# Kernel tuning notes

Measured on AMD Instinct MI355X. Metric: run time of the kernel, lower is better.

The kernel has to match this reference:

```python
import jax, jax.numpy as jnp
import numpy as np

N, E = 30000, 480000
IN_DIM, HID, HEADS, OUT_DIM, EDIM = 128, 64, 4, 32, 1
NEG_SLOPE = 0.2
EPS_BN = 1e-5


def segment_softmax(logits, seg, num_segments):
    m = jax.ops.segment_max(logits, seg, num_segments=num_segments)
    ex = jnp.exp(logits - m[seg])
    s = jax.ops.segment_sum(ex, seg, num_segments=num_segments)
    return ex / (s[seg] + 1e-16)


def gat_layer(x, src, dst, ea, W, We, a_s, a_d, a_e, b):
    # PyG GATConv: shared lin for src/dst, edge_dim attention, softmax over dst
    n = x.shape[0]
    H, D = a_s.shape
    h = (x @ W).reshape(n, H, D)                      # [N,H,D]
    e = (ea @ We).reshape(-1, H, D)                   # [E,H,D]
    logits = (h * a_s).sum(-1)[src] + (h * a_d).sum(-1)[dst] + (e * a_e).sum(-1)
    alpha = segment_softmax(jax.nn.leaky_relu(logits, NEG_SLOPE), dst, n)  # [E,H]
    out = jax.ops.segment_sum(alpha[:, :, None] * h[src], dst, num_segments=n)
    return out.reshape(n, H * D) + b


def setup_inputs() -> dict:
    key = jax.random.key(0)
    ks = jax.random.split(key, 24)
    s = 0.1
    return {
        "x": jax.random.normal(ks[0], (N, IN_DIM), jnp.float32),
        "edge_attr": jax.random.uniform(ks[1], (E, EDIM), jnp.float32),
        "bn_gamma": jnp.ones((EDIM,), jnp.float32),
        "bn_beta": jnp.zeros((EDIM,), jnp.float32),
        "W1": s * jax.random.normal(ks[2], (IN_DIM, HEADS * HID), jnp.float32),
        "We1": s * jax.random.normal(ks[3], (EDIM, HEADS * HID), jnp.float32),
        "a_src1": s * jax.random.normal(ks[4], (HEADS, HID), jnp.float32),
        "a_dst1": s * jax.random.normal(ks[5], (HEADS, HID), jnp.float32),
        "a_edge1": s * jax.random.normal(ks[6], (HEADS, HID), jnp.float32),
        "b1": jnp.zeros((HEADS * HID,), jnp.float32),
        "W2": s * jax.random.normal(ks[7], (HEADS * HID, OUT_DIM), jnp.float32),
        "We2": s * jax.random.normal(ks[8], (EDIM, OUT_DIM), jnp.float32),
        "a_src2": s * jax.random.normal(ks[9], (1, OUT_DIM), jnp.float32),
        "a_dst2": s * jax.random.normal(ks[10], (1, OUT_DIM), jnp.float32),
        "a_edge2": s * jax.random.normal(ks[11], (1, OUT_DIM), jnp.float32),
        "b2": jnp.zeros((OUT_DIM,), jnp.float32),
        "dec_W1": s * jax.random.normal(ks[12], (OUT_DIM, HID), jnp.float32),
        "dec_b1": jnp.zeros((HID,), jnp.float32),
        "dec_W2": s * jax.random.normal(ks[13], (HID, IN_DIM), jnp.float32),
        "dec_b2": jnp.zeros((IN_DIM,), jnp.float32),
        "edge_index": jax.random.randint(ks[14], (2, E), 0, N, dtype=jnp.int32),
    }


def reference(x, edge_attr, bn_gamma, bn_beta, W1, We1, a_src1, a_dst1, a_edge1, b1,
              W2, We2, a_src2, a_dst2, a_edge2, b2, dec_W1, dec_b1, dec_W2, dec_b2,
              edge_index):
    n = x.shape[0]
    src, dst = edge_index[0], edge_index[1]
    # BatchNorm1d (batch stats, biased var) on log1p(edge_attr)
    ea = jnp.log1p(edge_attr)
    mu = ea.mean(0)
    var = ea.var(0)
    ea = (ea - mu) / jnp.sqrt(var + EPS_BN) * bn_gamma + bn_beta
    # add_self_loops with fill_value='mean' (mean of incoming edge attrs per node)
    ones = jnp.ones((src.shape[0],), ea.dtype)
    cnt = jax.ops.segment_sum(ones, dst, num_segments=n)
    loop_attr = jax.ops.segment_sum(ea, dst, num_segments=n) / jnp.maximum(cnt, 1.0)[:, None]
    ar = jnp.arange(n)
    src2 = jnp.concatenate([src, ar])
    dst2 = jnp.concatenate([dst, ar])
    ea2 = jnp.concatenate([ea, loop_attr], axis=0)
    # encoder: 2-layer GAT (eval mode: dropout is identity)
    h = jax.nn.elu(gat_layer(x, src2, dst2, ea2, W1, We1, a_src1, a_dst1, a_edge1, b1))
    z = gat_layer(h, src2, dst2, ea2, W2, We2, a_src2, a_dst2, a_edge2, b2)
    # feature decoder MLP
    x_hat = jax.nn.elu(z @ dec_W1 + dec_b1) @ dec_W2 + dec_b2
    return z, x_hat
```

## Files before the change

### kernel.cpp

```cpp
#include <hip/hip_runtime.h>
#include <math.h>

#define NN 30000
#define EE 480000
#define NEG_SLOPE 0.2f
#define LDK 136
#define LDK2 264
#define CAP 48
#define NPB 1875
#define NGB 938
#define EAQ 32767.0f
#define LN2V 0.6931472f

static const size_t I_FILL  = 0;
static const size_t F_PART  = 30000;
static const size_t F_SCAL  = 34096;
static const size_t F_WTB   = 34112;
static const size_t F_WT2B  = 50496;
static const size_t F_HB    = 54592;
static const size_t F_S1    = 3894592;
static const size_t F_D1    = 4014592;
static const size_t F_H1B   = 4134592;
static const size_t F_H2    = 7974592;
static const size_t F_S2    = 8934592;
static const size_t F_D2    = 8964592;
static const size_t I_ER    = 8994592;

typedef __attribute__((ext_vector_type(4))) float f32x4;
typedef __attribute__((ext_vector_type(8))) short bf16x8;

__device__ __forceinline__ float wsum64(float v) {
    #pragma unroll
    for (int o = 32; o; o >>= 1) v += __shfl_xor(v, o);
    return v;
}
__device__ __forceinline__ unsigned int pack_bf2(float a, float b) {
    unsigned int ua = __float_as_uint(a);
    unsigned int ub = __float_as_uint(b);
    ua = (ua + 0x7FFFu + ((ua >> 16) & 1u)) >> 16;
    ub = (ub + 0x7FFFu + ((ub >> 16) & 1u)) & 0xFFFF0000u;
    return ua | ub;
}
__device__ __forceinline__ unsigned short bf16r(float f) {
    unsigned int u = __float_as_uint(f);
    u = (u + 0x7FFFu + ((u >> 16) & 1u)) >> 16;
    return (unsigned short)u;
}
__device__ __forceinline__ float bflo(unsigned int u) { return __uint_as_float(u << 16); }
__device__ __forceinline__ float bfhi(unsigned int u) { return __uint_as_float(u & 0xFFFF0000u); }

__global__ __launch_bounds__(256) void k_prepw(const float* __restrict__ W1,
        const float* __restrict__ W2, unsigned short* __restrict__ wtb,
        unsigned short* __restrict__ wt2b, int* __restrict__ fill) {
    int idx = blockIdx.x * 256 + threadIdx.x;
    if (idx < NN) fill[idx] = 0;
    if (idx < 128 * 256) {
        int k = idx >> 8, n = idx & 255;
        wtb[n * 128 + k] = bf16r(W1[idx]);
    } else if (idx < 128 * 256 + 256 * 32) {
        int i2 = idx - 128 * 256;
        int k = i2 >> 5, c = i2 & 31;
        wt2b[c * 256 + k] = bf16r(W2[i2]);
    }
}

__global__ __launch_bounds__(256) void k_scat_gemm(const int* __restrict__ src,
        const int* __restrict__ dst, const float* __restrict__ eattr,
        int* __restrict__ fill, unsigned int* __restrict__ er,
        float* __restrict__ part,
        const float* __restrict__ x, const unsigned short* __restrict__ wtb,
        const float* __restrict__ as1, const float* __restrict__ ad1,
        unsigned short* __restrict__ hb, float* __restrict__ s1,
        float* __restrict__ d1, int E, int M) {
    __shared__ char shbuf[32 * LDK * 2];
    int tid = threadIdx.x;

    if (blockIdx.x < NPB) {
        float* sa = (float*)shbuf;
        float* sb = sa + 256;
        int e = blockIdx.x * 256 + tid;
        float s = 0.f, s2 = 0.f;
        if (e < E) {
            float lv = log1pf(eattr[e]);
            s = lv; s2 = lv * lv;
            int d = dst[e];
            int pos = atomicAdd(&fill[d], 1);
            if (pos > CAP - 2) pos = CAP - 2;
            unsigned int q = (unsigned int)(lv * (EAQ / LN2V) + 0.5f);
            if (q > 32767u) q = 32767u;
            er[d * CAP + pos] = ((unsigned int)src[e] << 15) | q;
        }
        sa[tid] = s; sb[tid] = s2;
        __syncthreads();
        for (int o = 128; o; o >>= 1) {
            if (tid < o) { sa[tid] += sa[tid + o]; sb[tid] += sb[tid + o]; }
            __syncthreads();
        }
        if (tid == 0) { part[blockIdx.x * 2] = sa[0]; part[blockIdx.x * 2 + 1] = sb[0]; }
        return;
    }

    unsigned short* xs = (unsigned short*)shbuf;
    int bm = (blockIdx.x - NPB) * 32;
    #pragma unroll
    for (int i = 0; i < 4; i++) {
        int idx = tid + i * 256;
        int row = idx >> 5, c4 = (idx & 31) * 4;
        int grow = bm + row;
        float4 v = make_float4(0.f, 0.f, 0.f, 0.f);
        if (grow < M) v = *(const float4*)&x[grow * 128 + c4];
        uint2 p = make_uint2(pack_bf2(v.x, v.y), pack_bf2(v.z, v.w));
        *(uint2*)&xs[row * LDK + c4] = p;
    }
    __syncthreads();

    int w = tid >> 6;
    int l = tid & 63;
    int l15 = l & 15, lg = l >> 4;

    f32x4 acc[2][4];
    #pragma unroll
    for (int m = 0; m < 2; m++)
        #pragma unroll
        for (int n = 0; n < 4; n++) acc[m][n] = (f32x4){0.f, 0.f, 0.f, 0.f};

    #pragma unroll
    for (int ks = 0; ks < 4; ks++) {
        int k0 = ks * 32 + lg * 8;
        bf16x8 a0 = *(const bf16x8*)&xs[(l15) * LDK + k0];
        bf16x8 a1 = *(const bf16x8*)&xs[(16 + l15) * LDK + k0];
        bf16x8 b[4];
        #pragma unroll
        for (int n = 0; n < 4; n++)
            b[n] = *(const bf16x8*)&wtb[(w * 64 + n * 16 + l15) * 128 + k0];
        #pragma unroll
        for (int n = 0; n < 4; n++) {
            acc[0][n] = __builtin_amdgcn_mfma_f32_16x16x32_bf16(a0, b[n], acc[0][n], 0, 0, 0);
            acc[1][n] = __builtin_amdgcn_mfma_f32_16x16x32_bf16(a1, b[n], acc[1][n], 0, 0, 0);
        }
    }

    #pragma unroll
    for (int m = 0; m < 2; m++) {
        #pragma unroll
        for (int r = 0; r < 4; r++) {
            int grow = bm + m * 16 + lg * 4 + r;
            if (grow < M) {
                #pragma unroll
                for (int n = 0; n < 4; n++)
                    hb[grow * 256 + w * 64 + n * 16 + l15] = bf16r(acc[m][n][r]);
            }
        }
    }
    float as_c[4], ad_c[4];
    #pragma unroll
    for (int n = 0; n < 4; n++) {
        as_c[n] = as1[w * 64 + n * 16 + l15];
        ad_c[n] = ad1[w * 64 + n * 16 + l15];
    }
    float sp[2][4], dp[2][4];
    #pragma unroll
    for (int m = 0; m < 2; m++)
        #pragma unroll
        for (int r = 0; r < 4; r++) {
            float s = 0.f, d = 0.f;
            #pragma unroll
            for (int n = 0; n < 4; n++) {
                s += acc[m][n][r] * as_c[n];
                d += acc[m][n][r] * ad_c[n];
            }
            sp[m][r] = s; dp[m][r] = d;
        }
    #pragma unroll
    for (int o = 1; o < 16; o <<= 1) {
        #pragma unroll
        for (int m = 0; m < 2; m++)
            #pragma unroll
            for (int r = 0; r < 4; r++) {
                sp[m][r] += __shfl_xor(sp[m][r], o);
                dp[m][r] += __shfl_xor(dp[m][r], o);
            }
    }
    if (l15 == 0) {
        #pragma unroll
        for (int m = 0; m < 2; m++)
            #pragma unroll
            for (int r = 0; r < 4; r++) {
                int grow = bm + m * 16 + lg * 4 + r;
                if (grow < M) {
                    s1[grow * 4 + w] = sp[m][r];
                    d1[grow * 4 + w] = dp[m][r];
                }
            }
    }
}

__global__ __launch_bounds__(512) void k_bn_final(const float* __restrict__ part,
        const float* __restrict__ gamma, const float* __restrict__ beta,
        const float* __restrict__ We1, const float* __restrict__ ae1,
        const float* __restrict__ We2, const float* __restrict__ ae2,
        float* __restrict__ scal, int E) {
    __shared__ float sa[512], sb[512], sc[256];
    int tid = threadIdx.x;
    float s = 0.f, s2 = 0.f;
    for (int i = tid; i < NPB; i += 512) {
        s += part[2 * i]; s2 += part[2 * i + 1];
    }
    sa[tid] = s; sb[tid] = s2;
    if (tid < 256) sc[tid] = We1[tid] * ae1[tid];
    __syncthreads();
    for (int o = 256; o; o >>= 1) {
        if (tid < o) { sa[tid] += sa[tid + o]; sb[tid] += sb[tid + o]; }
        __syncthreads();
    }
    if (tid == 0) {
        float mu = sa[0] / (float)E;
        float var = sb[0] / (float)E - mu * mu;
        float kA = gamma[0] / sqrtf(var + 1e-5f);
        float kB = beta[0] - mu * kA;
        for (int h = 0; h < 4; h++) {
            float s1 = 0.f;
            for (int d = 0; d < 64; d++) s1 += sc[h * 64 + d];
            scal[4 + h] = kA * s1;
            scal[10 + h] = kB * s1;
        }
        float s22 = 0.f;
        for (int d = 0; d < 32; d++) s22 += We2[d] * ae2[d];
        scal[8] = kA * s22;
        scal[9] = kB * s22;
    }
}

__global__ __launch_bounds__(256) void k_agg1(const int* __restrict__ fill,
        const unsigned int* __restrict__ er, const float* __restrict__ s1,
        const float* __restrict__ d1, const float* __restrict__ scal,
        const unsigned short* __restrict__ hb, const float* __restrict__ b1,
        unsigned short* __restrict__ h1b, int N) {
    __shared__ float sma[4][256];
    __shared__ int   sms[4][64];
    int wid = threadIdx.x >> 6;
    int node = blockIdx.x * 4 + wid;
    if (node >= N) return;
    int lane = threadIdx.x & 63;
    int deg = fill[node]; if (deg > CAP - 1) deg = CAP - 1;
    float4 dv = *(const float4*)&d1[node * 4];
    float4 ce = *(const float4*)&scal[4];
    float4 cc = *(const float4*)&scal[10];

    unsigned int rec = (unsigned int)node << 15;
    if (lane < deg) rec = er[node * CAP + lane];
    unsigned int sidx = rec >> 15;
    float ev = (float)(rec & 32767u) * (LN2V / EAQ);
    if (lane >= deg) ev = 0.f;
    float evm = wsum64(ev) / fmaxf((float)deg, 1.f);
    int degT = deg + 1;
    if (lane == deg) ev = evm;
    bool valid = lane < degT;

    float4 l = make_float4(-1e30f, -1e30f, -1e30f, -1e30f);
    if (valid) {
        float4 sv = *(const float4*)&s1[sidx * 4];
        l.x = sv.x + dv.x + ev * ce.x + cc.x;
        l.y = sv.y + dv.y + ev * ce.y + cc.y;
        l.z = sv.z + dv.z + ev * ce.z + cc.z;
        l.w = sv.w + dv.w + ev * ce.w + cc.w;
        l.x = l.x > 0.f ? l.x : NEG_SLOPE * l.x;
        l.y = l.y > 0.f ? l.y : NEG_SLOPE * l.y;
        l.z = l.z > 0.f ? l.z : NEG_SLOPE * l.z;
        l.w = l.w > 0.f ? l.w : NEG_SLOPE * l.w;
    }
    float4 mx = l;
    #pragma unroll
    for (int o = 32; o; o >>= 1) {
        mx.x = fmaxf(mx.x, __shfl_xor(mx.x, o));
        mx.y = fmaxf(mx.y, __shfl_xor(mx.y, o));
        mx.z = fmaxf(mx.z, __shfl_xor(mx.z, o));
        mx.w = fmaxf(mx.w, __shfl_xor(mx.w, o));
    }
    float4 ex = make_float4(0.f, 0.f, 0.f, 0.f);
    if (valid) {
        ex.x = __expf(l.x - mx.x); ex.y = __expf(l.y - mx.y);
        ex.z = __expf(l.z - mx.z); ex.w = __expf(l.w - mx.w);
    }
    float4 sm = ex;
    #pragma unroll
    for (int o = 32; o; o >>= 1) {
        sm.x += __shfl_xor(sm.x, o); sm.y += __shfl_xor(sm.y, o);
        sm.z += __shfl_xor(sm.z, o); sm.w += __shfl_xor(sm.w, o);
    }
    *(float4*)&sma[wid][lane * 4] = make_float4(ex.x, ex.y, ex.z, ex.w);
    sms[wid][lane] = (int)sidx;
    int p = lane >> 5;
    int dL = lane & 31;
    int h = dL >> 3;
    float acc[8];
    #pragma unroll
    for (int i = 0; i < 8; i++) acc[i] = 0.f;
    for (int c0 = 0; c0 < degT; c0 += 8) {
        int sv[4]; float av[4];
        #pragma unroll
        for (int t = 0; t < 4; t++) {
            int ee = c0 + 2 * t + p;
            sv[t] = sms[wid][ee];
            av[t] = sma[wid][ee * 4 + h];
        }
        uint4 hv[4];
        #pragma unroll
        for (int t = 0; t < 4; t++)
            hv[t] = *(const uint4*)&hb[(unsigned)sv[t] * 256 + dL * 8];
        #pragma unroll
        for (int t = 0; t < 4; t++) {
            float a = av[t];
            acc[0] += a * bflo(hv[t].x); acc[1] += a * bfhi(hv[t].x);
            acc[2] += a * bflo(hv[t].y); acc[3] += a * bfhi(hv[t].y);
            acc[4] += a * bflo(hv[t].z); acc[5] += a * bfhi(hv[t].z);
            acc[6] += a * bflo(hv[t].w); acc[7] += a * bfhi(hv[t].w);
        }
    }
    #pragma unroll
    for (int i = 0; i < 8; i++) acc[i] += __shfl_xor(acc[i], 32);
    float smh = h == 0 ? sm.x : h == 1 ? sm.y : h == 2 ? sm.z : sm.w;
    float invh = 1.f / (smh + 1e-16f);
    float4 bb0 = *(const float4*)&b1[dL * 8];
    float4 bb1 = *(const float4*)&b1[dL * 8 + 4];
    float r[8];
    r[0] = acc[0] * invh + bb0.x; r[1] = acc[1] * invh + bb0.y;
    r[2] = acc[2] * invh + bb0.z; r[3] = acc[3] * invh + bb0.w;
    r[4] = acc[4] * invh + bb1.x; r[5] = acc[5] * invh + bb1.y;
    r[6] = acc[6] * invh + bb1.z; r[7] = acc[7] * invh + bb1.w;
    #pragma unroll
    for (int i = 0; i < 8; i++)
        r[i] = r[i] > 0.f ? r[i] : (__expf(r[i]) - 1.f);
    if (p == 0) {
        uint4 pk;
        pk.x = pack_bf2(r[0], r[1]); pk.y = pack_bf2(r[2], r[3]);
        pk.z = pack_bf2(r[4], r[5]); pk.w = pack_bf2(r[6], r[7]);
        *(uint4*)&h1b[node * 256 + dL * 8] = pk;
    }
}

__global__ __launch_bounds__(256) void k_gemm2(const unsigned short* __restrict__ h1b,
        const unsigned short* __restrict__ wt2b, const float* __restrict__ as2,
        const float* __restrict__ ad2, float* __restrict__ h2,
        float* __restrict__ s2, float* __restrict__ d2, int M) {
    __shared__ unsigned short h1s[64 * LDK2];
    __shared__ unsigned short w2s[32 * LDK2];
    int tid = threadIdx.x;
    int bm = blockIdx.x * 64;
    #pragma unroll
    for (int i = 0; i < 8; i++) {
        int c = tid + i * 256;
        int row = c >> 5, off = (c & 31) * 8;
        int grow = bm + row;
        uint4 v = make_uint4(0u, 0u, 0u, 0u);
        if (grow < M) v = *(const uint4*)&h1b[grow * 256 + off];
        *(uint4*)&h1s[row * LDK2 + off] = v;
    }
    #pragma unroll
    for (int i = 0; i < 4; i++) {
        int c = tid + i * 256;
        int row = c >> 5, off = (c & 31) * 8;
        uint4 v = *(const uint4*)&wt2b[row * 256 + off];
        *(uint4*)&w2s[row * LDK2 + off] = v;
    }
    __syncthreads();

    int w = tid >> 6;
    int l = tid & 63;
    int l15 = l & 15, lg = l >> 4;

    f32x4 acc0 = (f32x4){0.f, 0.f, 0.f, 0.f};
    f32x4 acc1 = (f32x4){0.f, 0.f, 0.f, 0.f};
    #pragma unroll
    for (int ks = 0; ks < 8; ks++) {
        int k0 = ks * 32 + lg * 8;
        bf16x8 a = *(const bf16x8*)&h1s[(w * 16 + l15) * LDK2 + k0];
        bf16x8 b0 = *(const bf16x8*)&w2s[(l15) * LDK2 + k0];
        bf16x8 b1 = *(const bf16x8*)&w2s[(16 + l15) * LDK2 + k0];
        acc0 = __builtin_amdgcn_mfma_f32_16x16x32_bf16(a, b0, acc0, 0, 0, 0);
        acc1 = __builtin_amdgcn_mfma_f32_16x16x32_bf16(a, b1, acc1, 0, 0, 0);
    }

    #pragma unroll
    for (int r = 0; r < 4; r++) {
        int grow = bm + w * 16 + lg * 4 + r;
        if (grow < M) {
            h2[grow * 32 + l15] = acc0[r];
            h2[grow * 32 + 16 + l15] = acc1[r];
        }
    }
    float sc0 = as2[l15], sc1 = as2[16 + l15];
    float dc0 = ad2[l15], dc1 = ad2[16 + l15];
    #pragma unroll
    for (int r = 0; r < 4; r++) {
        float sp = acc0[r] * sc0 + acc1[r] * sc1;
        float dp = acc0[r] * dc0 + acc1[r] * dc1;
        #pragma unroll
        for (int o = 1; o < 16; o <<= 1) {
            sp += __shfl_xor(sp, o);
            dp += __shfl_xor(dp, o);
        }
        if (l15 == 0) {
            int grow = bm + w * 16 + lg * 4 + r;
            if (grow < M) { s2[grow] = sp; d2[grow] = dp; }
        }
    }
}

__global__ __launch_bounds__(256) void k_agg2(const int* __restrict__ fill,
        const unsigned int* __restrict__ er, const float* __restrict__ s2,
        const float* __restrict__ d2, const float* __restrict__ scal,
        const float* __restrict__ h2, const float* __restrict__ b2,
        float* __restrict__ zout, int N) {
    __shared__ float sa2[4][64];
    __shared__ int   ss2[4][64];
    int wid = threadIdx.x >> 6;
    int node = blockIdx.x * 4 + wid;
    if (node >= N) return;
    int lane = threadIdx.x & 63;
    int deg = fill[node]; if (deg > CAP - 1) deg = CAP - 1;
    float dn = d2[node];
    float ce = scal[8], cc = scal[9];

    unsigned int rec = (unsigned int)node << 15;
    if (lane < deg) rec = er[node * CAP + lane];
    unsigned int sidx = rec >> 15;
    float ev = (float)(rec & 32767u) * (LN2V / EAQ);
    if (lane >= deg) ev = 0.f;
    float evm = wsum64(ev) / fmaxf((float)deg, 1.f);
    int degT = deg + 1;
    if (lane == deg) ev = evm;
    bool valid = lane < degT;

    float l = -1e30f;
    if (valid) {
        l = s2[sidx] + dn + ev * ce + cc;
        l = l > 0.f ? l : NEG_SLOPE * l;
    }
    float mx = l;
    #pragma unroll
    for (int o = 32; o; o >>= 1) mx = fmaxf(mx, __shfl_xor(mx, o));
    float ex = valid ? __expf(l - mx) : 0.f;
    float sm = wsum64(ex);
    float inv = 1.f / (sm + 1e-16f);
    sa2[wid][lane] = ex;
    ss2[wid][lane] = (int)sidx;
    int p8 = lane >> 3, dL2 = lane & 7;
    float4 acc = make_float4(0.f, 0.f, 0.f, 0.f);
    for (int c0 = 0; c0 < degT; c0 += 32) {
        int sv[4]; float av[4];
        #pragma unroll
        for (int t = 0; t < 4; t++) {
            int ee = c0 + 8 * t + p8;
            sv[t] = ss2[wid][ee];
            av[t] = sa2[wid][ee];
        }
        float4 hv[4];
        #pragma unroll
        for (int t = 0; t < 4; t++)
            hv[t] = *(const float4*)&h2[(unsigned)sv[t] * 32 + dL2 * 4];
        #pragma unroll
        for (int t = 0; t < 4; t++) {
            acc.x += av[t] * hv[t].x; acc.y += av[t] * hv[t].y;
            acc.z += av[t] * hv[t].z; acc.w += av[t] * hv[t].w;
        }
    }
    #pragma unroll
    for (int o = 8; o <= 32; o <<= 1) {
        acc.x += __shfl_xor(acc.x, o); acc.y += __shfl_xor(acc.y, o);
        acc.z += __shfl_xor(acc.z, o); acc.w += __shfl_xor(acc.w, o);
    }
    if (lane < 8) {
        float4 bb = *(const float4*)&b2[dL2 * 4];
        float4 oo;
        oo.x = acc.x * inv + bb.x; oo.y = acc.y * inv + bb.y;
        oo.z = acc.z * inv + bb.z; oo.w = acc.w * inv + bb.w;
        *(float4*)&zout[node * 32 + dL2 * 4] = oo;
    }
}

__global__ __launch_bounds__(256) void k_decoder(const float* __restrict__ z,
        const float* __restrict__ W1, const float* __restrict__ b1,
        const float* __restrict__ W2, const float* __restrict__ b2,
        float* __restrict__ xhat, int M) {
    __shared__ float zs[16][32];
    __shared__ float w1s[32 * 64];
    __shared__ float hid[16][68];
    __shared__ float w2s[64 * 128];
    int tid = threadIdx.x;
    int bn = blockIdx.x * 16;
    #pragma unroll
    for (int i = 0; i < 2; i++) {
        int idx = tid + i * 256;
        int r = idx >> 5, c = idx & 31;
        int row = bn + r;
        zs[r][c] = (row < M) ? z[row * 32 + c] : 0.f;
    }
    #pragma unroll
    for (int i = 0; i < 2; i++) {
        int idx = tid + i * 256;
        int r = idx >> 4, c = (idx & 15) * 4;
        *(float4*)&w1s[r * 64 + c] = *(const float4*)&W1[r * 64 + c];
    }
    #pragma unroll
    for (int i = 0; i < 8; i++) {
        int idx = tid + i * 256;
        int r = idx >> 5, c = (idx & 31) * 4;
        *(float4*)&w2s[r * 128 + c] = *(const float4*)&W2[r * 128 + c];
    }
    __syncthreads();
    {
        int nl = tid >> 4, c0 = (tid & 15) * 4;
        float4 acc = make_float4(0.f, 0.f, 0.f, 0.f);
        #pragma unroll 8
        for (int k = 0; k < 32; k++) {
            float zv = zs[nl][k];
            float4 w = *(float4*)&w1s[k * 64 + c0];
            acc.x += zv * w.x; acc.y += zv * w.y;
            acc.z += zv * w.z; acc.w += zv * w.w;
        }
        float4 bb = *(const float4*)&b1[c0];
        float r0 = acc.x + bb.x, r1 = acc.y + bb.y, r2 = acc.z + bb.z, r3 = acc.w + bb.w;
        r0 = r0 > 0.f ? r0 : (__expf(r0) - 1.f);
        r1 = r1 > 0.f ? r1 : (__expf(r1) - 1.f);
        r2 = r2 > 0.f ? r2 : (__expf(r2) - 1.f);
        r3 = r3 > 0.f ? r3 : (__expf(r3) - 1.f);
        hid[nl][c0] = r0; hid[nl][c0 + 1] = r1; hid[nl][c0 + 2] = r2; hid[nl][c0 + 3] = r3;
    }
    __syncthreads();
    {
        int nl = tid >> 4, c0 = (tid & 15) * 4;
        float acc[8];
        #pragma unroll
        for (int q = 0; q < 8; q++) acc[q] = 0.f;
        #pragma unroll 8
        for (int k = 0; k < 64; k++) {
            float hv = hid[nl][k];
            float4 w0 = *(float4*)&w2s[k * 128 + c0];
            float4 w1 = *(float4*)&w2s[k * 128 + c0 + 64];
            acc[0] += hv * w0.x; acc[1] += hv * w0.y; acc[2] += hv * w0.z; acc[3] += hv * w0.w;
            acc[4] += hv * w1.x; acc[5] += hv * w1.y; acc[6] += hv * w1.z; acc[7] += hv * w1.w;
        }
        int row = bn + nl;
        if (row < M) {
            float4 bb0 = *(const float4*)&b2[c0];
            float4 bb1 = *(const float4*)&b2[c0 + 64];
            float4 o0 = make_float4(acc[0] + bb0.x, acc[1] + bb0.y, acc[2] + bb0.z, acc[3] + bb0.w);
            float4 o1 = make_float4(acc[4] + bb1.x, acc[5] + bb1.y, acc[6] + bb1.z, acc[7] + bb1.w);
            *(float4*)&xhat[row * 128 + c0] = o0;
            *(float4*)&xhat[row * 128 + c0 + 64] = o1;
        }
    }
}

extern "C" void kernel_launch(void* const* d_in, const int* in_sizes, int n_in,
                              void* d_out, int out_size, void* d_ws, size_t ws_size,
                              hipStream_t stream) {
    const float* x        = (const float*)d_in[0];
    const float* eattr    = (const float*)d_in[1];
    const float* bn_gamma = (const float*)d_in[2];
    const float* bn_beta  = (const float*)d_in[3];
    const float* W1       = (const float*)d_in[4];
    const float* We1      = (const float*)d_in[5];
    const float* as1      = (const float*)d_in[6];
    const float* ad1      = (const float*)d_in[7];
    const float* ae1      = (const float*)d_in[8];
    const float* b1       = (const float*)d_in[9];
    const float* W2       = (const float*)d_in[10];
    const float* We2      = (const float*)d_in[11];
    const float* as2      = (const float*)d_in[12];
    const float* ad2      = (const float*)d_in[13];
    const float* ae2      = (const float*)d_in[14];
    const float* b2       = (const float*)d_in[15];
    const float* dW1      = (const float*)d_in[16];
    const float* db1      = (const float*)d_in[17];
    const float* dW2      = (const float*)d_in[18];
    const float* db2      = (const float*)d_in[19];
    const int*   eidx     = (const int*)d_in[20];
    const int* src = eidx;
    const int* dst = eidx + EE;

    float* ws = (float*)d_ws;
    int*   fill = (int*)(ws + I_FILL);
    float* part = ws + F_PART;
    float* scal = ws + F_SCAL;
    unsigned short* wtb  = (unsigned short*)(ws + F_WTB);
    unsigned short* wt2b = (unsigned short*)(ws + F_WT2B);
    unsigned short* hb   = (unsigned short*)(ws + F_HB);
    float* s1   = ws + F_S1;
    float* d1   = ws + F_D1;
    unsigned short* h1b = (unsigned short*)(ws + F_H1B);
    float* h2   = ws + F_H2;
    float* s2   = ws + F_S2;
    float* d2   = ws + F_D2;
    unsigned int* er = (unsigned int*)(ws + I_ER);

    float* zout = (float*)d_out;
    float* xhat = (float*)d_out + NN * 32;

    k_prepw<<<160, 256, 0, stream>>>(W1, W2, wtb, wt2b, fill);
    k_scat_gemm<<<NPB + NGB, 256, 0, stream>>>(src, dst, eattr, fill, er, part,
                                               x, wtb, as1, ad1, hb, s1, d1, EE, NN);
    k_bn_final<<<1, 512, 0, stream>>>(part, bn_gamma, bn_beta, We1, ae1, We2, ae2, scal, EE);
    k_agg1<<<(NN + 3) / 4, 256, 0, stream>>>(fill, er, s1, d1, scal, hb, b1, h1b, NN);
    k_gemm2<<<(NN + 63) / 64, 256, 0, stream>>>(h1b, wt2b, as2, ad2, h2, s2, d2, NN);
    k_agg2<<<(NN + 3) / 4, 256, 0, stream>>>(fill, er, s2, d2, scal, h2, b2, zout, NN);
    k_decoder<<<(NN + 15) / 16, 256, 0, stream>>>(zout, dW1, db1, dW2, db2, xhat, NN);
}
```

Before: 138.2 us.

## Partition edge scatter by destination mod 8 to keep atomics XCD-local

The scatter phase now launches 8 blocks per 2048-edge window, and each block handles only edges whose destination node falls in its residue class mod 8. Blocks are dispatched round-robin across the 8 XCDs, so the atomics on each fill counter stay within one XCD's L2. The fill counters are laid out per residue class so each XCD touches a contiguous slice. In exchange, every block reads dst for 8x as many edges and discards seven eighths of them, and the idea depends on the hardware mapping blocks to XCDs by blockIdx mod 8.

```diff
diff --git a/kernel.cpp b/kernel.cpp
--- a/kernel.cpp
+++ b/kernel.cpp
@@ -7,10 +7,12 @@
 #define LDK 136
 #define LDK2 264
 #define CAP 48
-#define NPB 1875
+#define NWIN 235
+#define NPB8 (NWIN * 8)
 #define NGB 938
 #define EAQ 32767.0f
 #define LN2V 0.6931472f
+#define FILL_IDX(d) (((d) & 7) * 3750 + ((d) >> 3))
 
 static const size_t I_FILL  = 0;
 static const size_t F_PART  = 30000;
@@ -75,20 +77,28 @@
     __shared__ char shbuf[32 * LDK * 2];
     int tid = threadIdx.x;
 
-    if (blockIdx.x < NPB) {
+    if (blockIdx.x < NPB8) {
         float* sa = (float*)shbuf;
         float* sb = sa + 256;
-        int e = blockIdx.x * 256 + tid;
+        int window = blockIdx.x >> 3;
+        int xcd = blockIdx.x & 7;
+        int base = window * 2048;
         float s = 0.f, s2 = 0.f;
-        if (e < E) {
-            float lv = log1pf(eattr[e]);
-            s = lv; s2 = lv * lv;
-            int d = dst[e];
-            int pos = atomicAdd(&fill[d], 1);
-            if (pos > CAP - 2) pos = CAP - 2;
-            unsigned int q = (unsigned int)(lv * (EAQ / LN2V) + 0.5f);
-            if (q > 32767u) q = 32767u;
-            er[d * CAP + pos] = ((unsigned int)src[e] << 15) | q;
+        #pragma unroll
+        for (int t = 0; t < 8; t++) {
+            int e = base + t * 256 + tid;
+            if (e < E) {
+                int d = dst[e];
+                if ((d & 7) == xcd) {
+                    float lv = log1pf(eattr[e]);
+                    s += lv; s2 += lv * lv;
+                    int pos = atomicAdd(&fill[FILL_IDX(d)], 1);
+                    if (pos > CAP - 2) pos = CAP - 2;
+                    unsigned int q = (unsigned int)(lv * (EAQ / LN2V) + 0.5f);
+                    if (q > 32767u) q = 32767u;
+                    er[d * CAP + pos] = ((unsigned int)src[e] << 15) | q;
+                }
+            }
         }
         sa[tid] = s; sb[tid] = s2;
         __syncthreads();
@@ -101,7 +111,7 @@
     }
 
     unsigned short* xs = (unsigned short*)shbuf;
-    int bm = (blockIdx.x - NPB) * 32;
+    int bm = (blockIdx.x - NPB8) * 32;
     #pragma unroll
     for (int i = 0; i < 4; i++) {
         int idx = tid + i * 256;
@@ -203,7 +213,7 @@
     __shared__ float sa[512], sb[512], sc[256];
     int tid = threadIdx.x;
     float s = 0.f, s2 = 0.f;
-    for (int i = tid; i < NPB; i += 512) {
+    for (int i = tid; i < NPB8; i += 512) {
         s += part[2 * i]; s2 += part[2 * i + 1];
     }
     sa[tid] = s; sb[tid] = s2;
@@ -242,7 +252,7 @@
     int node = blockIdx.x * 4 + wid;
     if (node >= N) return;
     int lane = threadIdx.x & 63;
-    int deg = fill[node]; if (deg > CAP - 1) deg = CAP - 1;
+    int deg = fill[FILL_IDX(node)]; if (deg > CAP - 1) deg = CAP - 1;
     float4 dv = *(const float4*)&d1[node * 4];
     float4 ce = *(const float4*)&scal[4];
     float4 cc = *(const float4*)&scal[10];
@@ -418,7 +428,7 @@
     int node = blockIdx.x * 4 + wid;
     if (node >= N) return;
     int lane = threadIdx.x & 63;
-    int deg = fill[node]; if (deg > CAP - 1) deg = CAP - 1;
+    int deg = fill[FILL_IDX(node)]; if (deg > CAP - 1) deg = CAP - 1;
     float dn = d2[node];
     float ce = scal[8], cc = scal[9];
 
@@ -599,8 +609,8 @@
     float* xhat = (float*)d_out + NN * 32;
 
     k_prepw<<<160, 256, 0, stream>>>(W1, W2, wtb, wt2b, fill);
-    k_scat_gemm<<<NPB + NGB, 256, 0, stream>>>(src, dst, eattr, fill, er, part,
-                                               x, wtb, as1, ad1, hb, s1, d1, EE, NN);
+    k_scat_gemm<<<NPB8 + NGB, 256, 0, stream>>>(src, dst, eattr, fill, er, part,
+                                                x, wtb, as1, ad1, hb, s1, d1, EE, NN);
     k_bn_final<<<1, 512, 0, stream>>>(part, bn_gamma, bn_beta, We1, ae1, We2, ae2, scal, EE);
     k_agg1<<<(NN + 3) / 4, 256, 0, stream>>>(fill, er, s1, d1, scal, hb, b1, h1b, NN);
     k_gemm2<<<(NN + 63) / 64, 256, 0, stream>>>(h1b, wt2b, as2, ad2, h2, s2, d2, NN);
```

After: 130.6 us (median of 2 runs). 1.06x faster.
